# Kernel tuning notes

Hardware: AMD Instinct MI355X
Metric: run time of the kernel (lower is better)

Reference implementation:

```python
import jax, jax.numpy as jnp
import numpy as np

N_NODES = 100000
N_EDGES = 1600000
IN_DIM = 128
OUT_DIM = 64


def setup_inputs() -> dict:
    key = jax.random.key(0)
    k1, k2, k3, k4 = jax.random.split(key, 4)
    x = jax.random.normal(k1, (N_NODES, IN_DIM), dtype=jnp.float32)
    edge_index = jax.random.randint(k2, (2, N_EDGES), 0, N_NODES, dtype=jnp.int32)
    edge_weight = jax.random.uniform(k3, (N_EDGES,), dtype=jnp.float32)
    weight = jax.random.normal(k4, (IN_DIM, OUT_DIM), dtype=jnp.float32) * (1.414 / np.sqrt(IN_DIM))
    bias = jnp.zeros((OUT_DIM,), dtype=jnp.float32)
    return {"x": x, "edge_index": edge_index, "edge_weight": edge_weight,
            "weight": weight, "bias": bias}


def reference(x, edge_index, edge_weight, weight, bias):
    # Dense transform: [N, in] @ [in, out] -> [N, out]
    h = jnp.matmul(x, weight)
    # Sparse aggregation (spmm): out[dst] += w_e * h[src]
    dst, src = edge_index[0], edge_index[1]
    msgs = edge_weight[:, None] * h[src]           # [E, out]
    out = jax.ops.segment_sum(msgs, dst, num_segments=N_NODES)
    return out + bias
```

## Files before the change

### kernel.cpp

```cpp
#include <hip/hip_runtime.h>

#define IN_DIM 128
#define OUT_DIM 64
#define PADF 36

static inline size_t align_up(size_t v, size_t a) { return (v + a - 1) & ~(a - 1); }

__global__ __launch_bounds__(256, 8) void gemm_block(
    const float* __restrict__ x, const float* __restrict__ w,
    float* __restrict__ h, int nrows) {
  __shared__ float xt[64 * PADF];
  const int tid = threadIdx.x;
  const int lane = tid & 63;
  const int wv = __builtin_amdgcn_readfirstlane(tid >> 6);
  const int rb = blockIdx.x * 64;

  float acc[16];
#pragma unroll
  for (int c = 0; c < 16; ++c) acc[c] = 0.f;

  const int r = tid >> 3;
  const int kq = (tid & 7) << 2;
  const float* wbase = w + wv * 16;

#pragma unroll 1
  for (int kc = 0; kc < IN_DIM; kc += 32) {
#pragma unroll
    for (int p = 0; p < 2; ++p) {
      int row = rb + r + p * 32;
      float4 v = (row < nrows)
                     ? *reinterpret_cast<const float4*>(x + (size_t)row * IN_DIM + kc + kq)
                     : make_float4(0.f, 0.f, 0.f, 0.f);
      *reinterpret_cast<float4*>(&xt[(r + p * 32) * PADF + kq]) = v;
    }
    __syncthreads();
#pragma unroll
    for (int k4 = 0; k4 < 32; k4 += 4) {
      float4 xv = *reinterpret_cast<const float4*>(&xt[lane * PADF + k4]);
#pragma unroll
      for (int kk = 0; kk < 4; ++kk) {
        float xs = (&xv.x)[kk];
        const float* wk = wbase + (size_t)(kc + k4 + kk) * OUT_DIM;
#pragma unroll
        for (int c = 0; c < 16; ++c)
          acc[c] = fmaf(xs, wk[c], acc[c]);
      }
    }
    __syncthreads();
  }

  int row = rb + lane;
  if (row < nrows) {
    float4* hp = reinterpret_cast<float4*>(h + (size_t)row * OUT_DIM + wv * 16);
#pragma unroll
    for (int c4 = 0; c4 < 4; ++c4)
      hp[c4] = make_float4(acc[c4 * 4], acc[c4 * 4 + 1], acc[c4 * 4 + 2], acc[c4 * 4 + 3]);
  }
}


__global__ __launch_bounds__(256) void zero_i32(int* __restrict__ p, int n) {
  int tid = blockIdx.x * blockDim.x + threadIdx.x;
  int stride = gridDim.x * blockDim.x;
  for (int i = tid; i < n; i += stride) p[i] = 0;
}

__global__ __launch_bounds__(256) void hist_kernel(
    const int* __restrict__ dst, int nedges, int* __restrict__ counts) {
  int tid = blockIdx.x * blockDim.x + threadIdx.x;
  int stride = gridDim.x * blockDim.x;
  for (int e = tid; e < nedges; e += stride) atomicAdd(&counts[dst[e]], 1);
}

__global__ __launch_bounds__(1024) void scan_block(
    const int* __restrict__ counts, int n, int* __restrict__ offsets,
    int* __restrict__ bsums) {
  __shared__ int buf[1024];
  int gid = blockIdx.x * 1024 + threadIdx.x;
  int v = (gid < n) ? counts[gid] : 0;
  buf[threadIdx.x] = v;
  __syncthreads();
  for (int d = 1; d < 1024; d <<= 1) {
    int t = (threadIdx.x >= d) ? buf[threadIdx.x - d] : 0;
    __syncthreads();
    buf[threadIdx.x] += t;
    __syncthreads();
  }
  if (gid < n) offsets[gid] = buf[threadIdx.x] - v;
  if (threadIdx.x == 1023) bsums[blockIdx.x] = buf[1023];
}

__global__ void scan_bsums(int* __restrict__ bsums, int nb) {
  if (threadIdx.x == 0 && blockIdx.x == 0) {
    int run = 0;
    for (int i = 0; i < nb; ++i) { int v = bsums[i]; bsums[i] = run; run += v; }
  }
}

__global__ __launch_bounds__(256) void add_bsums(
    int* __restrict__ offsets, const int* __restrict__ bsums, int n,
    int* __restrict__ cursor, int nnodes) {
  int tid = blockIdx.x * blockDim.x + threadIdx.x;
  int stride = gridDim.x * blockDim.x;
  for (int i = tid; i < n; i += stride) {
    int o = offsets[i] + bsums[i >> 10];
    offsets[i] = o;
    if (i < nnodes) cursor[i] = o;
  }
}

__global__ __launch_bounds__(256) void fill_part_kernel(
    const int* __restrict__ ei, const float* __restrict__ ew, int nedges,
    int* __restrict__ cursor, int2* __restrict__ csr, int nnodes) {
  const int range = blockIdx.x & 7;
  const int ngroups = gridDim.x >> 3;
  const int group = blockIdx.x >> 3;
  const int lo = (int)((size_t)range * nnodes / 8);
  const int hi = (int)((size_t)(range + 1) * nnodes / 8);
  int tid = group * blockDim.x + threadIdx.x;
  int stride = ngroups * blockDim.x;
  for (int e = tid; e < nedges; e += stride) {
    int d = ei[e];
    if (d >= lo && d < hi) {
      int s = ei[nedges + e];
      float wv = ew[e];
      int p = atomicAdd(&cursor[d], 1);
      csr[p] = make_int2(s, __float_as_int(wv));
    }
  }
}

__global__ __launch_bounds__(256) void gather_kernel(
    const int* __restrict__ offsets, const int2* __restrict__ csr,
    const float* __restrict__ h, const float* __restrict__ bias,
    float* __restrict__ out, int nnodes) {
  const int lane = threadIdx.x & 63;
  const int wid = blockIdx.x * (blockDim.x >> 6) + (threadIdx.x >> 6);
  const int nw = gridDim.x * (blockDim.x >> 6);
  const float b = bias[lane];

  for (int node = wid; node < nnodes; node += nw) {
    int beg = offsets[node];
    int end = offsets[node + 1];
    float acc = 0.f;
    for (int eo = beg; eo < end; eo += 64) {
      int cnt = min(64, end - eo);
      int2 me = (lane < cnt) ? csr[eo + lane] : make_int2(0, 0);
      int ms = me.x;
      float mw = __int_as_float(me.y);
      for (int j = 0; j < cnt; j += 8) {
        int s0 = __shfl(ms, j + 0), s1 = __shfl(ms, j + 1);
        int s2 = __shfl(ms, j + 2), s3 = __shfl(ms, j + 3);
        int s4 = __shfl(ms, j + 4), s5 = __shfl(ms, j + 5);
        int s6 = __shfl(ms, j + 6), s7 = __shfl(ms, j + 7);
        float w0 = __shfl(mw, j + 0), w1 = __shfl(mw, j + 1);
        float w2 = __shfl(mw, j + 2), w3 = __shfl(mw, j + 3);
        float w4 = __shfl(mw, j + 4), w5 = __shfl(mw, j + 5);
        float w6 = __shfl(mw, j + 6), w7 = __shfl(mw, j + 7);
        float h0 = h[(size_t)s0 * OUT_DIM + lane];
        float h1 = h[(size_t)s1 * OUT_DIM + lane];
        float h2 = h[(size_t)s2 * OUT_DIM + lane];
        float h3 = h[(size_t)s3 * OUT_DIM + lane];
        float h4 = h[(size_t)s4 * OUT_DIM + lane];
        float h5 = h[(size_t)s5 * OUT_DIM + lane];
        float h6 = h[(size_t)s6 * OUT_DIM + lane];
        float h7 = h[(size_t)s7 * OUT_DIM + lane];
        acc = fmaf(w0, h0, acc);
        acc = fmaf(w1, h1, acc);
        acc = fmaf(w2, h2, acc);
        acc = fmaf(w3, h3, acc);
        acc = fmaf(w4, h4, acc);
        acc = fmaf(w5, h5, acc);
        acc = fmaf(w6, h6, acc);
        acc = fmaf(w7, h7, acc);
      }
    }
    out[(size_t)node * OUT_DIM + lane] = acc + b;
  }
}

extern "C" void kernel_launch(void* const* d_in, const int* in_sizes, int n_in,
                              void* d_out, int out_size, void* d_ws, size_t ws_size,
                              hipStream_t stream) {
  const float* x    = (const float*)d_in[0];
  const int*   ei   = (const int*)d_in[1];
  const float* ew   = (const float*)d_in[2];
  const float* w    = (const float*)d_in[3];
  const float* bias = (const float*)d_in[4];
  float* out = (float*)d_out;

  const int nrows  = in_sizes[0] / IN_DIM;
  const int nedges = in_sizes[2];
  const int nscan  = nrows + 1;
  const int nblk   = (nscan + 1023) / 1024;

  char* ws = (char*)d_ws;
  size_t o = 0;
  float* h = (float*)(ws + o);           o += align_up((size_t)nrows * OUT_DIM * 4, 512);
  int* counts  = (int*)(ws + o);         o += align_up((size_t)nscan * 4, 512);
  int* offsets = (int*)(ws + o);         o += align_up((size_t)nscan * 4, 512);
  int* cursor  = (int*)(ws + o);         o += align_up((size_t)nrows * 4, 512);
  int* bsums   = (int*)(ws + o);         o += align_up((size_t)nblk * 4, 512);
  int2* csr    = (int2*)(ws + o);        o += align_up((size_t)nedges * 8, 512);

  hipLaunchKernelGGL(gemm_block, dim3((nrows + 63) / 64), dim3(256), 0, stream,
                     x, w, h, nrows);
  hipLaunchKernelGGL(zero_i32, dim3(128), dim3(256), 0, stream, counts, nscan);
  hipLaunchKernelGGL(hist_kernel, dim3(2048), dim3(256), 0, stream,
                     ei, nedges, counts);
  hipLaunchKernelGGL(scan_block, dim3(nblk), dim3(1024), 0, stream,
                     counts, nscan, offsets, bsums);
  hipLaunchKernelGGL(scan_bsums, dim3(1), dim3(64), 0, stream, bsums, nblk);
  hipLaunchKernelGGL(add_bsums, dim3(128), dim3(256), 0, stream,
                     offsets, bsums, nscan, cursor, nrows);
  hipLaunchKernelGGL(fill_part_kernel, dim3(2048), dim3(256), 0, stream,
                     ei, ew, nedges, cursor, csr, nrows);
  hipLaunchKernelGGL(gather_kernel, dim3(8192), dim3(256), 0, stream,
                     offsets, csr, h, bias, out, nrows);
}
```

Measured before the change: 335.4 us.

## Replace per-node CSR with 64-node bucket sort and LDS-accumulated gather

Replaces the per-node histogram, multi-kernel scan and CSR build with a coarse bucketing of edges into groups of 64 destination nodes. The histogram is done in LDS and the scan runs in a single block, and the destination's low bits are packed into the source index. The gather kernel gives one block per bucket and accumulates weighted rows into an LDS tile with shared-memory atomics before writing out. This cuts kernel launches, global atomic contention and scan cost. In exchange it adds LDS atomic contention, makes summation order nondeterministic, and relies on node ids fitting in 20 bits.

```diff
diff --git a/kernel.cpp b/kernel.cpp
--- a/kernel.cpp
+++ b/kernel.cpp
@@ -3,6 +3,9 @@
 #define IN_DIM 128
 #define OUT_DIM 64
 #define PADF 36
+#define BK_BITS 6
+#define BK_NODES 64
+#define CPAD 16
 
 static inline size_t align_up(size_t v, size_t a) { return (v + a - 1) & ~(a - 1); }
 
@@ -65,117 +68,132 @@
   for (int i = tid; i < n; i += stride) p[i] = 0;
 }
 
-__global__ __launch_bounds__(256) void hist_kernel(
-    const int* __restrict__ dst, int nedges, int* __restrict__ counts) {
-  int tid = blockIdx.x * blockDim.x + threadIdx.x;
+__global__ __launch_bounds__(256) void hist_lds_kernel(
+    const int* __restrict__ dst, int nedges, int* __restrict__ counts_pad,
+    int nb) {
+  __shared__ int hcnt[2048];
+  const int tid = threadIdx.x;
+  for (int i = tid; i < nb; i += 256) hcnt[i] = 0;
+  __syncthreads();
+  int gid = blockIdx.x * blockDim.x + tid;
   int stride = gridDim.x * blockDim.x;
-  for (int e = tid; e < nedges; e += stride) atomicAdd(&counts[dst[e]], 1);
-}
-
-__global__ __launch_bounds__(1024) void scan_block(
-    const int* __restrict__ counts, int n, int* __restrict__ offsets,
-    int* __restrict__ bsums) {
-  __shared__ int buf[1024];
-  int gid = blockIdx.x * 1024 + threadIdx.x;
-  int v = (gid < n) ? counts[gid] : 0;
-  buf[threadIdx.x] = v;
-  __syncthreads();
-  for (int d = 1; d < 1024; d <<= 1) {
-    int t = (threadIdx.x >= d) ? buf[threadIdx.x - d] : 0;
+  for (int e = gid; e < nedges; e += stride) {
+    int d = __builtin_nontemporal_load(dst + e);
+    atomicAdd(&hcnt[d >> BK_BITS], 1);
+  }
+  __syncthreads();
+  for (int i = tid; i < nb; i += 256) {
+    int v = hcnt[i];
+    if (v) atomicAdd(&counts_pad[i * CPAD], v);
+  }
+}
+
+__global__ __launch_bounds__(1024) void scan_buckets_kernel(
+    const int* __restrict__ counts_pad, int nb, int* __restrict__ offsets,
+    int* __restrict__ cursor_pad) {
+  __shared__ int sb[2][2048];
+  const int tid = threadIdx.x;
+  const int i0 = tid * 2, i1 = tid * 2 + 1;
+  sb[0][i0] = (i0 < nb) ? counts_pad[i0 * CPAD] : 0;
+  sb[0][i1] = (i1 < nb) ? counts_pad[i1 * CPAD] : 0;
+  __syncthreads();
+  int cur = 0;
+  for (int d = 1; d < 2048; d <<= 1) {
+    int a0 = sb[cur][i0] + ((i0 >= d) ? sb[cur][i0 - d] : 0);
+    int a1 = sb[cur][i1] + ((i1 >= d) ? sb[cur][i1 - d] : 0);
+    sb[cur ^ 1][i0] = a0;
+    sb[cur ^ 1][i1] = a1;
+    cur ^= 1;
     __syncthreads();
-    buf[threadIdx.x] += t;
-    __syncthreads();
-  }
-  if (gid < n) offsets[gid] = buf[threadIdx.x] - v;
-  if (threadIdx.x == 1023) bsums[blockIdx.x] = buf[1023];
-}
-
-__global__ void scan_bsums(int* __restrict__ bsums, int nb) {
-  if (threadIdx.x == 0 && blockIdx.x == 0) {
-    int run = 0;
-    for (int i = 0; i < nb; ++i) { int v = bsums[i]; bsums[i] = run; run += v; }
-  }
-}
-
-__global__ __launch_bounds__(256) void add_bsums(
-    int* __restrict__ offsets, const int* __restrict__ bsums, int n,
-    int* __restrict__ cursor, int nnodes) {
-  int tid = blockIdx.x * blockDim.x + threadIdx.x;
-  int stride = gridDim.x * blockDim.x;
-  for (int i = tid; i < n; i += stride) {
-    int o = offsets[i] + bsums[i >> 10];
-    offsets[i] = o;
-    if (i < nnodes) cursor[i] = o;
-  }
-}
-
-__global__ __launch_bounds__(256) void fill_part_kernel(
+  }
+  if (i0 <= nb) {
+    int e0 = (i0 == 0) ? 0 : sb[cur][i0 - 1];
+    offsets[i0] = e0;
+    if (i0 < nb) cursor_pad[i0 * CPAD] = e0;
+  }
+  if (i1 <= nb) {
+    int e1 = sb[cur][i1 - 1];
+    offsets[i1] = e1;
+    if (i1 < nb) cursor_pad[i1 * CPAD] = e1;
+  }
+}
+
+__global__ __launch_bounds__(256) void bucket_fill_kernel(
     const int* __restrict__ ei, const float* __restrict__ ew, int nedges,
-    int* __restrict__ cursor, int2* __restrict__ csr, int nnodes) {
+    int* __restrict__ cursor_pad, int2* __restrict__ bucketed, int nb) {
   const int range = blockIdx.x & 7;
   const int ngroups = gridDim.x >> 3;
   const int group = blockIdx.x >> 3;
-  const int lo = (int)((size_t)range * nnodes / 8);
-  const int hi = (int)((size_t)(range + 1) * nnodes / 8);
+  const int lo = (int)((size_t)range * nb / 8);
+  const int hi = (int)((size_t)(range + 1) * nb / 8);
   int tid = group * blockDim.x + threadIdx.x;
   int stride = ngroups * blockDim.x;
   for (int e = tid; e < nedges; e += stride) {
-    int d = ei[e];
-    if (d >= lo && d < hi) {
+    int d = __builtin_nontemporal_load(ei + e);
+    int b = d >> BK_BITS;
+    if (b >= lo && b < hi) {
       int s = ei[nedges + e];
       float wv = ew[e];
-      int p = atomicAdd(&cursor[d], 1);
-      csr[p] = make_int2(s, __float_as_int(wv));
-    }
-  }
-}
-
-__global__ __launch_bounds__(256) void gather_kernel(
-    const int* __restrict__ offsets, const int2* __restrict__ csr,
+      int p = atomicAdd(&cursor_pad[b * CPAD], 1);
+      bucketed[p] = make_int2(s | ((d & (BK_NODES - 1)) << 20),
+                              __float_as_int(wv));
+    }
+  }
+}
+
+__global__ __launch_bounds__(256) void lds_gather_kernel(
+    const int* __restrict__ offsets, const int2* __restrict__ bucketed,
     const float* __restrict__ h, const float* __restrict__ bias,
     float* __restrict__ out, int nnodes) {
-  const int lane = threadIdx.x & 63;
-  const int wid = blockIdx.x * (blockDim.x >> 6) + (threadIdx.x >> 6);
-  const int nw = gridDim.x * (blockDim.x >> 6);
-  const float b = bias[lane];
-
-  for (int node = wid; node < nnodes; node += nw) {
-    int beg = offsets[node];
-    int end = offsets[node + 1];
-    float acc = 0.f;
-    for (int eo = beg; eo < end; eo += 64) {
-      int cnt = min(64, end - eo);
-      int2 me = (lane < cnt) ? csr[eo + lane] : make_int2(0, 0);
-      int ms = me.x;
-      float mw = __int_as_float(me.y);
-      for (int j = 0; j < cnt; j += 8) {
-        int s0 = __shfl(ms, j + 0), s1 = __shfl(ms, j + 1);
-        int s2 = __shfl(ms, j + 2), s3 = __shfl(ms, j + 3);
-        int s4 = __shfl(ms, j + 4), s5 = __shfl(ms, j + 5);
-        int s6 = __shfl(ms, j + 6), s7 = __shfl(ms, j + 7);
-        float w0 = __shfl(mw, j + 0), w1 = __shfl(mw, j + 1);
-        float w2 = __shfl(mw, j + 2), w3 = __shfl(mw, j + 3);
-        float w4 = __shfl(mw, j + 4), w5 = __shfl(mw, j + 5);
-        float w6 = __shfl(mw, j + 6), w7 = __shfl(mw, j + 7);
-        float h0 = h[(size_t)s0 * OUT_DIM + lane];
-        float h1 = h[(size_t)s1 * OUT_DIM + lane];
-        float h2 = h[(size_t)s2 * OUT_DIM + lane];
-        float h3 = h[(size_t)s3 * OUT_DIM + lane];
-        float h4 = h[(size_t)s4 * OUT_DIM + lane];
-        float h5 = h[(size_t)s5 * OUT_DIM + lane];
-        float h6 = h[(size_t)s6 * OUT_DIM + lane];
-        float h7 = h[(size_t)s7 * OUT_DIM + lane];
-        acc = fmaf(w0, h0, acc);
-        acc = fmaf(w1, h1, acc);
-        acc = fmaf(w2, h2, acc);
-        acc = fmaf(w3, h3, acc);
-        acc = fmaf(w4, h4, acc);
-        acc = fmaf(w5, h5, acc);
-        acc = fmaf(w6, h6, acc);
-        acc = fmaf(w7, h7, acc);
-      }
-    }
-    out[(size_t)node * OUT_DIM + lane] = acc + b;
+  __shared__ float tile[BK_NODES * OUT_DIM];
+  const int tid = threadIdx.x;
+  const int lane = tid & 63;
+  const int wv = __builtin_amdgcn_readfirstlane(tid >> 6);
+  const int b = blockIdx.x;
+
+#pragma unroll
+  for (int i = 0; i < BK_NODES * OUT_DIM / 256; ++i)
+    tile[tid + i * 256] = 0.f;
+  __syncthreads();
+
+  const int beg = offsets[b];
+  const int end = offsets[b + 1];
+  const int cnt = end - beg;
+  const int per = (cnt + 3) >> 2;
+  int e = beg + wv * per;
+  const int wend = min(e + per, end);
+
+  for (; e + 4 <= wend; e += 4) {
+    int2 m0 = bucketed[e + 0];
+    int2 m1 = bucketed[e + 1];
+    int2 m2 = bucketed[e + 2];
+    int2 m3 = bucketed[e + 3];
+    float g0 = h[(size_t)(m0.x & 0xFFFFF) * OUT_DIM + lane];
+    float g1 = h[(size_t)(m1.x & 0xFFFFF) * OUT_DIM + lane];
+    float g2 = h[(size_t)(m2.x & 0xFFFFF) * OUT_DIM + lane];
+    float g3 = h[(size_t)(m3.x & 0xFFFFF) * OUT_DIM + lane];
+    atomicAdd(&tile[((m0.x >> 20) & 63) * OUT_DIM + lane], __int_as_float(m0.y) * g0);
+    atomicAdd(&tile[((m1.x >> 20) & 63) * OUT_DIM + lane], __int_as_float(m1.y) * g1);
+    atomicAdd(&tile[((m2.x >> 20) & 63) * OUT_DIM + lane], __int_as_float(m2.y) * g2);
+    atomicAdd(&tile[((m3.x >> 20) & 63) * OUT_DIM + lane], __int_as_float(m3.y) * g3);
+  }
+  for (; e < wend; ++e) {
+    int2 m = bucketed[e];
+    float g = h[(size_t)(m.x & 0xFFFFF) * OUT_DIM + lane];
+    atomicAdd(&tile[((m.x >> 20) & 63) * OUT_DIM + lane], __int_as_float(m.y) * g);
+  }
+  __syncthreads();
+
+  const float4* bias4 = reinterpret_cast<const float4*>(bias);
+  for (int i = tid; i < BK_NODES * 16; i += 256) {
+    int r = i >> 4, c4 = i & 15;
+    int node = (b << BK_BITS) + r;
+    if (node < nnodes) {
+      float4 t = *reinterpret_cast<const float4*>(&tile[r * OUT_DIM + c4 * 4]);
+      float4 bb = bias4[c4];
+      float4 o = make_float4(t.x + bb.x, t.y + bb.y, t.z + bb.z, t.w + bb.w);
+      *reinterpret_cast<float4*>(&out[(size_t)node * OUT_DIM + c4 * 4]) = o;
+    }
   }
 }
 
@@ -191,30 +209,26 @@
 
   const int nrows  = in_sizes[0] / IN_DIM;
   const int nedges = in_sizes[2];
-  const int nscan  = nrows + 1;
-  const int nblk   = (nscan + 1023) / 1024;
+  const int nb     = (nrows + BK_NODES - 1) >> BK_BITS;
 
   char* ws = (char*)d_ws;
   size_t o = 0;
-  float* h = (float*)(ws + o);           o += align_up((size_t)nrows * OUT_DIM * 4, 512);
-  int* counts  = (int*)(ws + o);         o += align_up((size_t)nscan * 4, 512);
-  int* offsets = (int*)(ws + o);         o += align_up((size_t)nscan * 4, 512);
-  int* cursor  = (int*)(ws + o);         o += align_up((size_t)nrows * 4, 512);
-  int* bsums   = (int*)(ws + o);         o += align_up((size_t)nblk * 4, 512);
-  int2* csr    = (int2*)(ws + o);        o += align_up((size_t)nedges * 8, 512);
+  float* h = (float*)(ws + o);            o += align_up((size_t)nrows * OUT_DIM * 4, 512);
+  int* counts_pad = (int*)(ws + o);       o += align_up((size_t)nb * CPAD * 4, 512);
+  int* cursor_pad = (int*)(ws + o);       o += align_up((size_t)nb * CPAD * 4, 512);
+  int* offsets    = (int*)(ws + o);       o += align_up((size_t)(nb + 1) * 4, 512);
+  int2* bucketed  = (int2*)(ws + o);      o += align_up((size_t)nedges * 8, 512);
 
   hipLaunchKernelGGL(gemm_block, dim3((nrows + 63) / 64), dim3(256), 0, stream,
                      x, w, h, nrows);
-  hipLaunchKernelGGL(zero_i32, dim3(128), dim3(256), 0, stream, counts, nscan);
-  hipLaunchKernelGGL(hist_kernel, dim3(2048), dim3(256), 0, stream,
-                     ei, nedges, counts);
-  hipLaunchKernelGGL(scan_block, dim3(nblk), dim3(1024), 0, stream,
-                     counts, nscan, offsets, bsums);
-  hipLaunchKernelGGL(scan_bsums, dim3(1), dim3(64), 0, stream, bsums, nblk);
-  hipLaunchKernelGGL(add_bsums, dim3(128), dim3(256), 0, stream,
-                     offsets, bsums, nscan, cursor, nrows);
-  hipLaunchKernelGGL(fill_part_kernel, dim3(2048), dim3(256), 0, stream,
-                     ei, ew, nedges, cursor, csr, nrows);
-  hipLaunchKernelGGL(gather_kernel, dim3(8192), dim3(256), 0, stream,
-                     offsets, csr, h, bias, out, nrows);
-}
+  hipLaunchKernelGGL(zero_i32, dim3(64), dim3(256), 0, stream,
+                     counts_pad, nb * CPAD);
+  hipLaunchKernelGGL(hist_lds_kernel, dim3(256), dim3(256), 0, stream,
+                     ei, nedges, counts_pad, nb);
+  hipLaunchKernelGGL(scan_buckets_kernel, dim3(1), dim3(1024), 0, stream,
+                     counts_pad, nb, offsets, cursor_pad);
+  hipLaunchKernelGGL(bucket_fill_kernel, dim3(2048), dim3(256), 0, stream,
+                     ei, ew, nedges, cursor_pad, bucketed, nb);
+  hipLaunchKernelGGL(lds_gather_kernel, dim3(nb), dim3(256), 0, stream,
+                     offsets, bucketed, h, bias, out, nrows);
+}
```

Result: slower. 837.8 us (+149.8%).
